# Kernel optimization log

Measured on AMD Instinct MI355X. Metric: run time of the kernel, lower is better.

## Reference

```python
import jax, jax.numpy as jnp
import numpy as np

B, T, D = 32, 512, 1024
EPS = 1e-12  # torch F.normalize eps


def smooth_l1(x):
    # nn.SmoothL1Loss default beta=1.0
    a = jnp.abs(x)
    return jnp.where(a < 1.0, 0.5 * x * x, a - 0.5)


def setup_inputs() -> dict:
    key = jax.random.key(0)
    k1, k2, k3, k4 = jax.random.split(key, 4)
    return {
        "word_targets": jax.random.normal(k1, (B, T, D), dtype=jnp.float32),
        "image_targets": jax.random.normal(k2, (B, D), dtype=jnp.float32),
        "preds": jax.random.normal(k3, (B, T, D), dtype=jnp.float32),
        "decode_lengths": jax.random.randint(k4, (B,), 1, T + 1, dtype=jnp.int32),
    }


def reference(word_targets, image_targets, preds, decode_lengths):
    # mask over valid (ragged) positions: [B, T]
    mask = (jnp.arange(T)[None, :] < decode_lengths[:, None]).astype(preds.dtype)
    lens = decode_lengths.astype(preds.dtype)  # [B]

    # word loss: per-sample mean of smooth_l1 over valid tokens x D
    sl1 = smooth_l1(preds - word_targets) * mask[:, :, None]  # [B,T,D]
    word_per_b = sl1.sum(axis=(1, 2)) / (lens * D)             # [B]
    word_loss = word_per_b.mean()

    # per-sentence means over valid tokens: [B, D]
    pred_mean = (preds * mask[:, :, None]).sum(axis=1) / lens[:, None]
    targ_mean = (word_targets * mask[:, :, None]).sum(axis=1) / lens[:, None]
    sentence_loss = smooth_l1(pred_mean - targ_mean).mean(axis=1).mean()

    # image embedding loss: compare pred sentence mean to L2-normalized image embedding
    norm = jnp.maximum(jnp.linalg.norm(image_targets, axis=-1, keepdims=True), EPS)
    img_norm = image_targets / norm
    image_loss = smooth_l1(pred_mean - img_norm).mean(axis=1).mean()

    return word_loss + sentence_loss + image_loss
```

## Files before the change

### kernel.cpp

```cpp
#include <hip/hip_runtime.h>
#include <math.h>

static constexpr int B_ = 32;
static constexpr int T_ = 512;
static constexpr int D_ = 1024;
static constexpr int NT_ = 32;
static constexpr int TCHUNK_ = T_ / NT_;
static constexpr float EPS_ = 1e-12f;

__device__ __forceinline__ float sl1f(float x) {
    float a = fabsf(x);
    return a < 1.0f ? 0.5f * x * x : a - 0.5f;
}

__device__ __forceinline__ float blockReduce256(float v, float* lds) {
#pragma unroll
    for (int o = 32; o > 0; o >>= 1) v += __shfl_down(v, o, 64);
    int wid = threadIdx.x >> 6, lane = threadIdx.x & 63;
    if (lane == 0) lds[wid] = v;
    __syncthreads();
    float tot = lds[0] + lds[1] + lds[2] + lds[3];
    __syncthreads();
    return tot;
}

__global__ __launch_bounds__(256) void pass1_kernel(
    const float* __restrict__ preds, const float* __restrict__ wtarg,
    const int* __restrict__ lens,
    float* __restrict__ wsPred, float* __restrict__ wsTarg, float* __restrict__ wsSl1)
{
    __shared__ float lds[4];
    const int c = blockIdx.x, b = blockIdx.y;
    const int len = lens[b];
    const int t0 = c * TCHUNK_;
    if (t0 >= len) return;
    const int nrows = min(TCHUNK_, len - t0);
    const int tid = threadIdx.x;

    const float4* pp = reinterpret_cast<const float4*>(preds)
                       + (size_t)(b * T_ + t0) * (D_ / 4) + tid;
    const float4* pw = reinterpret_cast<const float4*>(wtarg)
                       + (size_t)(b * T_ + t0) * (D_ / 4) + tid;

    float4 ps = make_float4(0.f, 0.f, 0.f, 0.f);
    float4 ts = make_float4(0.f, 0.f, 0.f, 0.f);
    float s = 0.f;

    if (nrows == TCHUNK_) {
#pragma unroll
        for (int t = 0; t < TCHUNK_; ++t) {
            float4 p = pp[(size_t)t * (D_ / 4)];
            float4 w = pw[(size_t)t * (D_ / 4)];
            ps.x += p.x; ps.y += p.y; ps.z += p.z; ps.w += p.w;
            ts.x += w.x; ts.y += w.y; ts.z += w.z; ts.w += w.w;
            s += sl1f(p.x - w.x) + sl1f(p.y - w.y) + sl1f(p.z - w.z) + sl1f(p.w - w.w);
        }
    } else {
        for (int t = 0; t < nrows; ++t) {
            float4 p = pp[(size_t)t * (D_ / 4)];
            float4 w = pw[(size_t)t * (D_ / 4)];
            ps.x += p.x; ps.y += p.y; ps.z += p.z; ps.w += p.w;
            ts.x += w.x; ts.y += w.y; ts.z += w.z; ts.w += w.w;
            s += sl1f(p.x - w.x) + sl1f(p.y - w.y) + sl1f(p.z - w.z) + sl1f(p.w - w.w);
        }
    }

    const size_t off = ((size_t)b * NT_ + c) * (D_ / 4) + tid;
    reinterpret_cast<float4*>(wsPred)[off] = ps;
    reinterpret_cast<float4*>(wsTarg)[off] = ts;

    float tot = blockReduce256(s, lds);
    if (tid == 0) wsSl1[b * NT_ + c] = tot;
}

__global__ __launch_bounds__(256) void pass2_kernel(
    const float* __restrict__ img, const int* __restrict__ lens,
    const float* __restrict__ wsPred, const float* __restrict__ wsTarg,
    const float* __restrict__ wsSl1, float* __restrict__ wsP)
{
    __shared__ float4 lA[8][32];
    __shared__ float4 lB[8][32];
    __shared__ float lred[4];

    const int g = blockIdx.x, b = blockIdx.y;
    const int tid = threadIdx.x;
    const int c8 = tid >> 5, j = tid & 31;
    const int len = lens[b];
    const float flen = (float)len;
    const int ntmax = (len + TCHUNK_ - 1) / TCHUNK_;

    const float4* img4 = reinterpret_cast<const float4*>(img);
    float4 im = img4[(size_t)b * (D_ / 4) + tid];
    float ss = im.x * im.x + im.y * im.y + im.z * im.z + im.w * im.w;
    float sumsq = blockReduce256(ss, lred);
    float inv_norm = 1.0f / fmaxf(sqrtf(sumsq), EPS_);

    float4 ap = make_float4(0.f, 0.f, 0.f, 0.f);
    float4 at = make_float4(0.f, 0.f, 0.f, 0.f);
#pragma unroll
    for (int k = 0; k < NT_ / 8; ++k) {
        int nt = c8 + k * 8;
        if (nt < ntmax) {
            size_t off = ((size_t)b * NT_ + nt) * (D_ / 4) + (size_t)g * 32 + j;
            float4 p = reinterpret_cast<const float4*>(wsPred)[off];
            float4 w = reinterpret_cast<const float4*>(wsTarg)[off];
            ap.x += p.x; ap.y += p.y; ap.z += p.z; ap.w += p.w;
            at.x += w.x; at.y += w.y; at.z += w.z; at.w += w.w;
        }
    }
    lA[c8][j] = ap;
    lB[c8][j] = at;
    __syncthreads();

    float part = 0.f;
    if (tid < 32) {
        float4 ps = make_float4(0.f, 0.f, 0.f, 0.f);
        float4 ts = make_float4(0.f, 0.f, 0.f, 0.f);
#pragma unroll
        for (int k = 0; k < 8; ++k) {
            float4 p = lA[k][tid], w = lB[k][tid];
            ps.x += p.x; ps.y += p.y; ps.z += p.z; ps.w += p.w;
            ts.x += w.x; ts.y += w.y; ts.z += w.z; ts.w += w.w;
        }
        const float pmx = ps.x / flen, pmy = ps.y / flen, pmz = ps.z / flen, pmw = ps.w / flen;
        const float tmx = ts.x / flen, tmy = ts.y / flen, tmz = ts.z / flen, tmw = ts.w / flen;
        float4 iv = img4[(size_t)b * (D_ / 4) + g * 32 + tid];
        part  = sl1f(pmx - tmx) + sl1f(pmy - tmy) + sl1f(pmz - tmz) + sl1f(pmw - tmw);
        part += sl1f(pmx - iv.x * inv_norm) + sl1f(pmy - iv.y * inv_norm)
              + sl1f(pmz - iv.z * inv_norm) + sl1f(pmw - iv.w * inv_norm);
    }
#pragma unroll
    for (int o = 16; o > 0; o >>= 1) part += __shfl_down(part, o, 64);

    if (tid == 0) {
        float wsum = 0.f;
#pragma unroll
        for (int k = 0; k < NT_ / 8; ++k) {
            int nt = g * (NT_ / 8) + k;
            if (nt < ntmax) wsum += wsSl1[b * NT_ + nt];
        }
        wsP[b * 8 + g] = part / (float)D_ + wsum / (flen * (float)D_);
    }
}

__global__ __launch_bounds__(256) void pass3_kernel(const float* __restrict__ wsP,
                                                    float* __restrict__ out)
{
    __shared__ float lred[4];
    float v = wsP[threadIdx.x];
    float tot = blockReduce256(v, lred);
    if (threadIdx.x == 0) out[0] = tot / (float)B_;
}

extern "C" void kernel_launch(void* const* d_in, const int* in_sizes, int n_in,
                              void* d_out, int out_size, void* d_ws, size_t ws_size,
                              hipStream_t stream) {
    const float* wtarg = (const float*)d_in[0];
    const float* img   = (const float*)d_in[1];
    const float* preds = (const float*)d_in[2];
    const int*   lens  = (const int*)d_in[3];
    float* out = (float*)d_out;

    float* wsPred = (float*)d_ws;
    float* wsTarg = wsPred + (size_t)B_ * NT_ * D_;
    float* wsSl1  = wsTarg + (size_t)B_ * NT_ * D_;
    float* wsP    = wsSl1 + (size_t)B_ * NT_;

    pass1_kernel<<<dim3(NT_, B_), 256, 0, stream>>>(preds, wtarg, lens, wsPred, wsTarg, wsSl1);
    pass2_kernel<<<dim3(8, B_), 256, 0, stream>>>(img, lens, wsPred, wsTarg, wsSl1, wsP);
    pass3_kernel<<<1, 256, 0, stream>>>(wsP, out);
}
```

Baseline: 25.92 us.

## Fuse pass2/pass3 into pass1 via last-block atomic counters, add prep kernel

Replaces the three-kernel pipeline with a small prep kernel, which computes the image inverse norms and zeroes the counters, and one fused kernel. In the fused kernel, the last block to finish for each sample (found through an atomic counter) reduces the chunk partials and computes the per-sample loss. The last sample to finish then does the final mean. This removes one launch and the pass2/pass3 grid overheads. In exchange, a single block per sample now serially reduces up to 32 chunk partials, and the fence/atomic synchronisation is added.

```diff
diff --git a/kernel.cpp b/kernel.cpp
--- a/kernel.cpp
+++ b/kernel.cpp
@@ -24,132 +24,129 @@
     return tot;
 }
 
-__global__ __launch_bounds__(256) void pass1_kernel(
+__global__ __launch_bounds__(256) void prep_kernel(const float* __restrict__ img,
+                                                   float* __restrict__ wsInvNorm,
+                                                   int* __restrict__ ctrs)
+{
+    __shared__ float lred[4];
+    const int b = blockIdx.x, tid = threadIdx.x;
+    if (tid == 0) ctrs[b] = 0;
+    if (b == 0 && tid == 1) ctrs[B_] = 0;
+
+    float4 iv = reinterpret_cast<const float4*>(img)[(size_t)b * (D_ / 4) + tid];
+    float ss = iv.x * iv.x + iv.y * iv.y + iv.z * iv.z + iv.w * iv.w;
+    float sumsq = blockReduce256(ss, lred);
+    if (tid == 0) wsInvNorm[b] = 1.0f / fmaxf(sqrtf(sumsq), EPS_);
+}
+
+__global__ __launch_bounds__(256) void fused_kernel(
     const float* __restrict__ preds, const float* __restrict__ wtarg,
-    const int* __restrict__ lens,
-    float* __restrict__ wsPred, float* __restrict__ wsTarg, float* __restrict__ wsSl1)
+    const float* __restrict__ img, const int* __restrict__ lens,
+    float* __restrict__ wsPred, float* __restrict__ wsTarg,
+    float* __restrict__ wsSl1, float* __restrict__ wsPerB,
+    const float* __restrict__ wsInvNorm, int* __restrict__ ctrs,
+    float* __restrict__ out)
 {
-    __shared__ float lds[4];
+    __shared__ float lred[4];
+    __shared__ int bcast;
     const int c = blockIdx.x, b = blockIdx.y;
     const int len = lens[b];
     const int t0 = c * TCHUNK_;
-    if (t0 >= len) return;
-    const int nrows = min(TCHUNK_, len - t0);
     const int tid = threadIdx.x;
 
-    const float4* pp = reinterpret_cast<const float4*>(preds)
-                       + (size_t)(b * T_ + t0) * (D_ / 4) + tid;
-    const float4* pw = reinterpret_cast<const float4*>(wtarg)
-                       + (size_t)(b * T_ + t0) * (D_ / 4) + tid;
+    if (t0 < len) {
+        const int nrows = min(TCHUNK_, len - t0);
+        const float4* pp = reinterpret_cast<const float4*>(preds)
+                           + (size_t)(b * T_ + t0) * (D_ / 4) + tid;
+        const float4* pw = reinterpret_cast<const float4*>(wtarg)
+                           + (size_t)(b * T_ + t0) * (D_ / 4) + tid;
+
+        float4 ps = make_float4(0.f, 0.f, 0.f, 0.f);
+        float4 ts = make_float4(0.f, 0.f, 0.f, 0.f);
+        float s = 0.f;
+
+        if (nrows == TCHUNK_) {
+#pragma unroll
+            for (int t = 0; t < TCHUNK_; ++t) {
+                float4 p = pp[(size_t)t * (D_ / 4)];
+                float4 w = pw[(size_t)t * (D_ / 4)];
+                ps.x += p.x; ps.y += p.y; ps.z += p.z; ps.w += p.w;
+                ts.x += w.x; ts.y += w.y; ts.z += w.z; ts.w += w.w;
+                s += sl1f(p.x - w.x) + sl1f(p.y - w.y) + sl1f(p.z - w.z) + sl1f(p.w - w.w);
+            }
+        } else {
+            for (int t = 0; t < nrows; ++t) {
+                float4 p = pp[(size_t)t * (D_ / 4)];
+                float4 w = pw[(size_t)t * (D_ / 4)];
+                ps.x += p.x; ps.y += p.y; ps.z += p.z; ps.w += p.w;
+                ts.x += w.x; ts.y += w.y; ts.z += w.z; ts.w += w.w;
+                s += sl1f(p.x - w.x) + sl1f(p.y - w.y) + sl1f(p.z - w.z) + sl1f(p.w - w.w);
+            }
+        }
+
+        const size_t off = ((size_t)b * NT_ + c) * (D_ / 4) + tid;
+        reinterpret_cast<float4*>(wsPred)[off] = ps;
+        reinterpret_cast<float4*>(wsTarg)[off] = ts;
+
+        float tot = blockReduce256(s, lred);
+        if (tid == 0) wsSl1[b * NT_ + c] = tot;
+    }
+
+    if (tid == 0) {
+        __threadfence();
+        bcast = atomicAdd(&ctrs[b], 1);
+    }
+    __syncthreads();
+    if (bcast != NT_ - 1) return;
+    __threadfence();
+
+    const float flen = (float)len;
+    const int ntmax = (len + TCHUNK_ - 1) / TCHUNK_;
 
     float4 ps = make_float4(0.f, 0.f, 0.f, 0.f);
     float4 ts = make_float4(0.f, 0.f, 0.f, 0.f);
-    float s = 0.f;
-
-    if (nrows == TCHUNK_) {
-#pragma unroll
-        for (int t = 0; t < TCHUNK_; ++t) {
-            float4 p = pp[(size_t)t * (D_ / 4)];
-            float4 w = pw[(size_t)t * (D_ / 4)];
-            ps.x += p.x; ps.y += p.y; ps.z += p.z; ps.w += p.w;
-            ts.x += w.x; ts.y += w.y; ts.z += w.z; ts.w += w.w;
-            s += sl1f(p.x - w.x) + sl1f(p.y - w.y) + sl1f(p.z - w.z) + sl1f(p.w - w.w);
-        }
-    } else {
-        for (int t = 0; t < nrows; ++t) {
-            float4 p = pp[(size_t)t * (D_ / 4)];
-            float4 w = pw[(size_t)t * (D_ / 4)];
-            ps.x += p.x; ps.y += p.y; ps.z += p.z; ps.w += p.w;
-            ts.x += w.x; ts.y += w.y; ts.z += w.z; ts.w += w.w;
-            s += sl1f(p.x - w.x) + sl1f(p.y - w.y) + sl1f(p.z - w.z) + sl1f(p.w - w.w);
-        }
+#pragma unroll 8
+    for (int nt = 0; nt < ntmax; ++nt) {
+        const size_t off = ((size_t)b * NT_ + nt) * (D_ / 4) + tid;
+        float4 p = reinterpret_cast<const float4*>(wsPred)[off];
+        float4 w = reinterpret_cast<const float4*>(wsTarg)[off];
+        ps.x += p.x; ps.y += p.y; ps.z += p.z; ps.w += p.w;
+        ts.x += w.x; ts.y += w.y; ts.z += w.z; ts.w += w.w;
     }
 
-    const size_t off = ((size_t)b * NT_ + c) * (D_ / 4) + tid;
-    reinterpret_cast<float4*>(wsPred)[off] = ps;
-    reinterpret_cast<float4*>(wsTarg)[off] = ts;
+    const float inv_norm = wsInvNorm[b];
+    float4 iv = reinterpret_cast<const float4*>(img)[(size_t)b * (D_ / 4) + tid];
 
-    float tot = blockReduce256(s, lds);
-    if (tid == 0) wsSl1[b * NT_ + c] = tot;
-}
+    const float pmx = ps.x / flen, pmy = ps.y / flen, pmz = ps.z / flen, pmw = ps.w / flen;
+    const float tmx = ts.x / flen, tmy = ts.y / flen, tmz = ts.z / flen, tmw = ts.w / flen;
 
-__global__ __launch_bounds__(256) void pass2_kernel(
-    const float* __restrict__ img, const int* __restrict__ lens,
-    const float* __restrict__ wsPred, const float* __restrict__ wsTarg,
-    const float* __restrict__ wsSl1, float* __restrict__ wsP)
-{
-    __shared__ float4 lA[8][32];
-    __shared__ float4 lB[8][32];
-    __shared__ float lred[4];
+    float s_bd = sl1f(pmx - tmx) + sl1f(pmy - tmy) + sl1f(pmz - tmz) + sl1f(pmw - tmw)
+               + sl1f(pmx - iv.x * inv_norm) + sl1f(pmy - iv.y * inv_norm)
+               + sl1f(pmz - iv.z * inv_norm) + sl1f(pmw - iv.w * inv_norm);
+    float tot = blockReduce256(s_bd, lred);
 
-    const int g = blockIdx.x, b = blockIdx.y;
-    const int tid = threadIdx.x;
-    const int c8 = tid >> 5, j = tid & 31;
-    const int len = lens[b];
-    const float flen = (float)len;
-    const int ntmax = (len + TCHUNK_ - 1) / TCHUNK_;
-
-    const float4* img4 = reinterpret_cast<const float4*>(img);
-    float4 im = img4[(size_t)b * (D_ / 4) + tid];
-    float ss = im.x * im.x + im.y * im.y + im.z * im.z + im.w * im.w;
-    float sumsq = blockReduce256(ss, lred);
-    float inv_norm = 1.0f / fmaxf(sqrtf(sumsq), EPS_);
-
-    float4 ap = make_float4(0.f, 0.f, 0.f, 0.f);
-    float4 at = make_float4(0.f, 0.f, 0.f, 0.f);
+    float wv = (tid < ntmax) ? wsSl1[b * NT_ + tid] : 0.f;
+    if (tid < 64) {
 #pragma unroll
-    for (int k = 0; k < NT_ / 8; ++k) {
-        int nt = c8 + k * 8;
-        if (nt < ntmax) {
-            size_t off = ((size_t)b * NT_ + nt) * (D_ / 4) + (size_t)g * 32 + j;
-            float4 p = reinterpret_cast<const float4*>(wsPred)[off];
-            float4 w = reinterpret_cast<const float4*>(wsTarg)[off];
-            ap.x += p.x; ap.y += p.y; ap.z += p.z; ap.w += p.w;
-            at.x += w.x; at.y += w.y; at.z += w.z; at.w += w.w;
-        }
+        for (int o = 32; o > 0; o >>= 1) wv += __shfl_down(wv, o, 64);
     }
-    lA[c8][j] = ap;
-    lB[c8][j] = at;
-    __syncthreads();
-
-    float part = 0.f;
-    if (tid < 32) {
-        float4 ps = make_float4(0.f, 0.f, 0.f, 0.f);
-        float4 ts = make_float4(0.f, 0.f, 0.f, 0.f);
-#pragma unroll
-        for (int k = 0; k < 8; ++k) {
-            float4 p = lA[k][tid], w = lB[k][tid];
-            ps.x += p.x; ps.y += p.y; ps.z += p.z; ps.w += p.w;
-            ts.x += w.x; ts.y += w.y; ts.z += w.z; ts.w += w.w;
-        }
-        const float pmx = ps.x / flen, pmy = ps.y / flen, pmz = ps.z / flen, pmw = ps.w / flen;
-        const float tmx = ts.x / flen, tmy = ts.y / flen, tmz = ts.z / flen, tmw = ts.w / flen;
-        float4 iv = img4[(size_t)b * (D_ / 4) + g * 32 + tid];
-        part  = sl1f(pmx - tmx) + sl1f(pmy - tmy) + sl1f(pmz - tmz) + sl1f(pmw - tmw);
-        part += sl1f(pmx - iv.x * inv_norm) + sl1f(pmy - iv.y * inv_norm)
-              + sl1f(pmz - iv.z * inv_norm) + sl1f(pmw - iv.w * inv_norm);
-    }
-#pragma unroll
-    for (int o = 16; o > 0; o >>= 1) part += __shfl_down(part, o, 64);
+    if (tid == 0)
+        wsPerB[b] = tot / (float)D_ + wv / (flen * (float)D_);
 
     if (tid == 0) {
-        float wsum = 0.f;
+        __threadfence();
+        bcast = atomicAdd(&ctrs[B_], 1);
+    }
+    __syncthreads();
+    if (bcast != B_ - 1) return;
+    __threadfence();
+
+    float v = (tid < B_) ? wsPerB[tid] : 0.f;
+    if (tid < 64) {
 #pragma unroll
-        for (int k = 0; k < NT_ / 8; ++k) {
-            int nt = g * (NT_ / 8) + k;
-            if (nt < ntmax) wsum += wsSl1[b * NT_ + nt];
-        }
-        wsP[b * 8 + g] = part / (float)D_ + wsum / (flen * (float)D_);
+        for (int o = 32; o > 0; o >>= 1) v += __shfl_down(v, o, 64);
     }
-}
-
-__global__ __launch_bounds__(256) void pass3_kernel(const float* __restrict__ wsP,
-                                                    float* __restrict__ out)
-{
-    __shared__ float lred[4];
-    float v = wsP[threadIdx.x];
-    float tot = blockReduce256(v, lred);
-    if (threadIdx.x == 0) out[0] = tot / (float)B_;
+    if (tid == 0) out[0] = v / (float)B_;
 }
 
 extern "C" void kernel_launch(void* const* d_in, const int* in_sizes, int n_in,
@@ -161,12 +158,14 @@
     const int*   lens  = (const int*)d_in[3];
     float* out = (float*)d_out;
 
-    float* wsPred = (float*)d_ws;
-    float* wsTarg = wsPred + (size_t)B_ * NT_ * D_;
-    float* wsSl1  = wsTarg + (size_t)B_ * NT_ * D_;
-    float* wsP    = wsSl1 + (size_t)B_ * NT_;
+    float* wsPred    = (float*)d_ws;
+    float* wsTarg    = wsPred + (size_t)B_ * NT_ * D_;
+    float* wsSl1     = wsTarg + (size_t)B_ * NT_ * D_;
+    float* wsPerB    = wsSl1 + (size_t)B_ * NT_;
+    float* wsInvNorm = wsPerB + B_;
+    int*   ctrs      = (int*)(wsInvNorm + B_);
 
-    pass1_kernel<<<dim3(NT_, B_), 256, 0, stream>>>(preds, wtarg, lens, wsPred, wsTarg, wsSl1);
-    pass2_kernel<<<dim3(8, B_), 256, 0, stream>>>(img, lens, wsPred, wsTarg, wsSl1, wsP);
-    pass3_kernel<<<1, 256, 0, stream>>>(wsP, out);
+    prep_kernel<<<B_, 256, 0, stream>>>(img, wsInvNorm, ctrs);
+    fused_kernel<<<dim3(NT_, B_), 256, 0, stream>>>(
+        preds, wtarg, img, lens, wsPred, wsTarg, wsSl1, wsPerB, wsInvNorm, ctrs, out);
 }
```

Result: slower. 89.92 us (+246.9%).

## Retile pass1 into larger time chunks with D-quarter split and fuse final reduction

Applied to the files above, without the earlier changes.

Pass1 now splits each sample into 4 time chunks and 4 feature quarters. Each block has four waves working on interleaved rows, reduces their partials in LDS, and issues 8-deep batched loads to keep more memory requests in flight. This shrinks the partial-sum workspace from 32 to 4 chunks, so pass2 reads less and becomes one block per sample that adds its result into the output with an atomic. The third kernel launch is removed. In exchange the float atomic makes summation order nondeterministic, out is zeroed inside pass1, and there are fewer blocks (512) to spread across CUs.

```diff
diff --git a/kernel.cpp b/kernel.cpp
--- a/kernel.cpp
+++ b/kernel.cpp
@@ -4,8 +4,9 @@
 static constexpr int B_ = 32;
 static constexpr int T_ = 512;
 static constexpr int D_ = 1024;
-static constexpr int NT_ = 32;
-static constexpr int TCHUNK_ = T_ / NT_;
+static constexpr int NCH_ = 4;
+static constexpr int TCH_ = T_ / NCH_;
+static constexpr int NDQ_ = 4;
 static constexpr float EPS_ = 1e-12f;
 
 __device__ __forceinline__ float sl1f(float x) {
@@ -24,70 +25,92 @@
     return tot;
 }
 
-__global__ __launch_bounds__(256) void pass1_kernel(
+__global__ __launch_bounds__(256, 2) void pass1_kernel(
     const float* __restrict__ preds, const float* __restrict__ wtarg,
     const int* __restrict__ lens,
-    float* __restrict__ wsPred, float* __restrict__ wsTarg, float* __restrict__ wsSl1)
+    float* __restrict__ wsPred, float* __restrict__ wsTarg,
+    float* __restrict__ wsSl1, float* __restrict__ out)
 {
-    __shared__ float lds[4];
-    const int c = blockIdx.x, b = blockIdx.y;
+    __shared__ float4 redP[4][64];
+    __shared__ float4 redT[4][64];
+    __shared__ float lred[4];
+
+    const int c = blockIdx.x, b = blockIdx.y, q = blockIdx.z;
+    const int tid = threadIdx.x;
+    if (c == 0 && b == 0 && q == 0 && tid == 0) out[0] = 0.f;
+
     const int len = lens[b];
-    const int t0 = c * TCHUNK_;
+    const int t0 = c * TCH_;
     if (t0 >= len) return;
-    const int nrows = min(TCHUNK_, len - t0);
-    const int tid = threadIdx.x;
+    const int nrows = min(TCH_, len - t0);
+
+    const int j = tid & 63;
+    const int r4 = tid >> 6;
 
     const float4* pp = reinterpret_cast<const float4*>(preds)
-                       + (size_t)(b * T_ + t0) * (D_ / 4) + tid;
+                       + (size_t)(b * T_ + t0) * (D_ / 4) + q * 64 + j;
     const float4* pw = reinterpret_cast<const float4*>(wtarg)
-                       + (size_t)(b * T_ + t0) * (D_ / 4) + tid;
+                       + (size_t)(b * T_ + t0) * (D_ / 4) + q * 64 + j;
 
     float4 ps = make_float4(0.f, 0.f, 0.f, 0.f);
     float4 ts = make_float4(0.f, 0.f, 0.f, 0.f);
     float s = 0.f;
 
-    if (nrows == TCHUNK_) {
+    if (nrows == TCH_) {
 #pragma unroll
-        for (int t = 0; t < TCHUNK_; ++t) {
-            float4 p = pp[(size_t)t * (D_ / 4)];
-            float4 w = pw[(size_t)t * (D_ / 4)];
-            ps.x += p.x; ps.y += p.y; ps.z += p.z; ps.w += p.w;
-            ts.x += w.x; ts.y += w.y; ts.z += w.z; ts.w += w.w;
-            s += sl1f(p.x - w.x) + sl1f(p.y - w.y) + sl1f(p.z - w.z) + sl1f(p.w - w.w);
+        for (int tt = 0; tt < 4; ++tt) {
+            float4 p[8], w[8];
+#pragma unroll
+            for (int jj = 0; jj < 8; ++jj)
+                p[jj] = pp[(size_t)(r4 + 4 * (tt * 8 + jj)) * (D_ / 4)];
+#pragma unroll
+            for (int jj = 0; jj < 8; ++jj)
+                w[jj] = pw[(size_t)(r4 + 4 * (tt * 8 + jj)) * (D_ / 4)];
+#pragma unroll
+            for (int jj = 0; jj < 8; ++jj) {
+                ps.x += p[jj].x; ps.y += p[jj].y; ps.z += p[jj].z; ps.w += p[jj].w;
+                ts.x += w[jj].x; ts.y += w[jj].y; ts.z += w[jj].z; ts.w += w[jj].w;
+                s += sl1f(p[jj].x - w[jj].x) + sl1f(p[jj].y - w[jj].y)
+                   + sl1f(p[jj].z - w[jj].z) + sl1f(p[jj].w - w[jj].w);
+            }
         }
     } else {
-        for (int t = 0; t < nrows; ++t) {
-            float4 p = pp[(size_t)t * (D_ / 4)];
-            float4 w = pw[(size_t)t * (D_ / 4)];
+        for (int r = r4; r < nrows; r += 4) {
+            float4 p = pp[(size_t)r * (D_ / 4)];
+            float4 w = pw[(size_t)r * (D_ / 4)];
             ps.x += p.x; ps.y += p.y; ps.z += p.z; ps.w += p.w;
             ts.x += w.x; ts.y += w.y; ts.z += w.z; ts.w += w.w;
             s += sl1f(p.x - w.x) + sl1f(p.y - w.y) + sl1f(p.z - w.z) + sl1f(p.w - w.w);
         }
     }
 
-    const size_t off = ((size_t)b * NT_ + c) * (D_ / 4) + tid;
-    reinterpret_cast<float4*>(wsPred)[off] = ps;
-    reinterpret_cast<float4*>(wsTarg)[off] = ts;
-
-    float tot = blockReduce256(s, lds);
-    if (tid == 0) wsSl1[b * NT_ + c] = tot;
+    redP[r4][j] = ps;
+    redT[r4][j] = ts;
+    float tot = blockReduce256(s, lred);
+    if (tid < 64) {
+        float4 a0 = redP[0][tid], a1 = redP[1][tid], a2 = redP[2][tid], a3 = redP[3][tid];
+        float4 ap = make_float4(a0.x + a1.x + a2.x + a3.x, a0.y + a1.y + a2.y + a3.y,
+                                a0.z + a1.z + a2.z + a3.z, a0.w + a1.w + a2.w + a3.w);
+        float4 b0 = redT[0][tid], b1 = redT[1][tid], b2 = redT[2][tid], b3 = redT[3][tid];
+        float4 at = make_float4(b0.x + b1.x + b2.x + b3.x, b0.y + b1.y + b2.y + b3.y,
+                                b0.z + b1.z + b2.z + b3.z, b0.w + b1.w + b2.w + b3.w);
+        const size_t off = ((size_t)(b * NCH_ + c)) * (D_ / 4) + q * 64 + tid;
+        reinterpret_cast<float4*>(wsPred)[off] = ap;
+        reinterpret_cast<float4*>(wsTarg)[off] = at;
+    }
+    if (tid == 0) wsSl1[(b * NCH_ + c) * NDQ_ + q] = tot;
 }
 
 __global__ __launch_bounds__(256) void pass2_kernel(
     const float* __restrict__ img, const int* __restrict__ lens,
     const float* __restrict__ wsPred, const float* __restrict__ wsTarg,
-    const float* __restrict__ wsSl1, float* __restrict__ wsP)
+    const float* __restrict__ wsSl1, float* __restrict__ out)
 {
-    __shared__ float4 lA[8][32];
-    __shared__ float4 lB[8][32];
     __shared__ float lred[4];
-
-    const int g = blockIdx.x, b = blockIdx.y;
-    const int tid = threadIdx.x;
-    const int c8 = tid >> 5, j = tid & 31;
+    const int b = blockIdx.x, tid = threadIdx.x;
     const int len = lens[b];
     const float flen = (float)len;
-    const int ntmax = (len + TCHUNK_ - 1) / TCHUNK_;
+    const int nc = (len + TCH_ - 1) / TCH_;
 
     const float4* img4 = reinterpret_cast<const float4*>(img);
     float4 im = img4[(size_t)b * (D_ / 4) + tid];
@@ -95,61 +118,41 @@
     float sumsq = blockReduce256(ss, lred);
     float inv_norm = 1.0f / fmaxf(sqrtf(sumsq), EPS_);
 
-    float4 ap = make_float4(0.f, 0.f, 0.f, 0.f);
-    float4 at = make_float4(0.f, 0.f, 0.f, 0.f);
+    float4 ps = make_float4(0.f, 0.f, 0.f, 0.f);
+    float4 ts = make_float4(0.f, 0.f, 0.f, 0.f);
 #pragma unroll
-    for (int k = 0; k < NT_ / 8; ++k) {
-        int nt = c8 + k * 8;
-        if (nt < ntmax) {
-            size_t off = ((size_t)b * NT_ + nt) * (D_ / 4) + (size_t)g * 32 + j;
+    for (int c = 0; c < NCH_; ++c) {
+        if (c < nc) {
+            const size_t off = ((size_t)(b * NCH_ + c)) * (D_ / 4) + tid;
             float4 p = reinterpret_cast<const float4*>(wsPred)[off];
             float4 w = reinterpret_cast<const float4*>(wsTarg)[off];
-            ap.x += p.x; ap.y += p.y; ap.z += p.z; ap.w += p.w;
-            at.x += w.x; at.y += w.y; at.z += w.z; at.w += w.w;
-        }
-    }
-    lA[c8][j] = ap;
-    lB[c8][j] = at;
-    __syncthreads();
-
-    float part = 0.f;
-    if (tid < 32) {
-        float4 ps = make_float4(0.f, 0.f, 0.f, 0.f);
-        float4 ts = make_float4(0.f, 0.f, 0.f, 0.f);
-#pragma unroll
-        for (int k = 0; k < 8; ++k) {
-            float4 p = lA[k][tid], w = lB[k][tid];
             ps.x += p.x; ps.y += p.y; ps.z += p.z; ps.w += p.w;
             ts.x += w.x; ts.y += w.y; ts.z += w.z; ts.w += w.w;
         }
-        const float pmx = ps.x / flen, pmy = ps.y / flen, pmz = ps.z / flen, pmw = ps.w / flen;
-        const float tmx = ts.x / flen, tmy = ts.y / flen, tmz = ts.z / flen, tmw = ts.w / flen;
-        float4 iv = img4[(size_t)b * (D_ / 4) + g * 32 + tid];
-        part  = sl1f(pmx - tmx) + sl1f(pmy - tmy) + sl1f(pmz - tmz) + sl1f(pmw - tmw);
-        part += sl1f(pmx - iv.x * inv_norm) + sl1f(pmy - iv.y * inv_norm)
-              + sl1f(pmz - iv.z * inv_norm) + sl1f(pmw - iv.w * inv_norm);
     }
+
+    const float pmx = ps.x / flen, pmy = ps.y / flen, pmz = ps.z / flen, pmw = ps.w / flen;
+    const float tmx = ts.x / flen, tmy = ts.y / flen, tmz = ts.z / flen, tmw = ts.w / flen;
+
+    float s = sl1f(pmx - tmx) + sl1f(pmy - tmy) + sl1f(pmz - tmz) + sl1f(pmw - tmw)
+            + sl1f(pmx - im.x * inv_norm) + sl1f(pmy - im.y * inv_norm)
+            + sl1f(pmz - im.z * inv_norm) + sl1f(pmw - im.w * inv_norm);
+    float tot = blockReduce256(s, lred);
+
+    float wv = 0.f;
+    if (tid < NCH_ * NDQ_) {
+        int c = tid >> 2;
+        if (c < nc) wv = wsSl1[(b * NCH_ + c) * NDQ_ + (tid & 3)];
+    }
+    if (tid < 64) {
 #pragma unroll
-    for (int o = 16; o > 0; o >>= 1) part += __shfl_down(part, o, 64);
+        for (int o = 32; o > 0; o >>= 1) wv += __shfl_down(wv, o, 64);
+    }
 
     if (tid == 0) {
-        float wsum = 0.f;
-#pragma unroll
-        for (int k = 0; k < NT_ / 8; ++k) {
-            int nt = g * (NT_ / 8) + k;
-            if (nt < ntmax) wsum += wsSl1[b * NT_ + nt];
-        }
-        wsP[b * 8 + g] = part / (float)D_ + wsum / (flen * (float)D_);
+        float per_b = tot / (float)D_ + wv / (flen * (float)D_);
+        atomicAdd(out, per_b * (1.0f / (float)B_));
     }
-}
-
-__global__ __launch_bounds__(256) void pass3_kernel(const float* __restrict__ wsP,
-                                                    float* __restrict__ out)
-{
-    __shared__ float lred[4];
-    float v = wsP[threadIdx.x];
-    float tot = blockReduce256(v, lred);
-    if (threadIdx.x == 0) out[0] = tot / (float)B_;
 }
 
 extern "C" void kernel_launch(void* const* d_in, const int* in_sizes, int n_in,
@@ -162,11 +165,10 @@
     float* out = (float*)d_out;
 
     float* wsPred = (float*)d_ws;
-    float* wsTarg = wsPred + (size_t)B_ * NT_ * D_;
-    float* wsSl1  = wsTarg + (size_t)B_ * NT_ * D_;
-    float* wsP    = wsSl1 + (size_t)B_ * NT_;
+    float* wsTarg = wsPred + (size_t)B_ * NCH_ * D_;
+    float* wsSl1  = wsTarg + (size_t)B_ * NCH_ * D_;
 
-    pass1_kernel<<<dim3(NT_, B_), 256, 0, stream>>>(preds, wtarg, lens, wsPred, wsTarg, wsSl1);
-    pass2_kernel<<<dim3(8, B_), 256, 0, stream>>>(img, lens, wsPred, wsTarg, wsSl1, wsP);
-    pass3_kernel<<<1, 256, 0, stream>>>(wsP, out);
+    pass1_kernel<<<dim3(NCH_, B_, NDQ_), 256, 0, stream>>>(
+        preds, wtarg, lens, wsPred, wsTarg, wsSl1, out);
+    pass2_kernel<<<B_, 256, 0, stream>>>(img, lens, wsPred, wsTarg, wsSl1, out);
 }
```

Result: slower. 28.66 us (+10.6%).
